# Kernel optimization log

Measured on AMD Instinct MI355X. Metric: run time of the kernel, lower is better.

## Reference

```python
import jax, jax.numpy as jnp
import numpy as np

CENTER_RADIUS = 2.5
TOPK = 13
IOU_WEIGHT = 3.0
BETA = 2.0
NUM_CLASSES = 80
BBOX_W = 2.0
BIG = 1e8
EPS = 1e-7
IMG = 1280


def pairwise_iou(boxes, gts):
    # boxes [N,4], gts [M,4] xyxy -> [N,M]
    lt = jnp.maximum(boxes[:, None, :2], gts[None, :, :2])
    rb = jnp.minimum(boxes[:, None, 2:], gts[None, :, 2:])
    wh = jnp.clip(rb - lt, 0.0)
    inter = wh[..., 0] * wh[..., 1]
    area_a = (boxes[:, 2] - boxes[:, 0]) * (boxes[:, 3] - boxes[:, 1])
    area_b = (gts[:, 2] - gts[:, 0]) * (gts[:, 3] - gts[:, 1])
    union = area_a[:, None] + area_b[None, :] - inter
    return inter / jnp.maximum(union, EPS)


def giou_elementwise(a, b):
    # a,b [N,4] xyxy -> [N]
    lt = jnp.maximum(a[:, :2], b[:, :2])
    rb = jnp.minimum(a[:, 2:], b[:, 2:])
    wh = jnp.clip(rb - lt, 0.0)
    inter = wh[:, 0] * wh[:, 1]
    area_a = (a[:, 2] - a[:, 0]) * (a[:, 3] - a[:, 1])
    area_b = (b[:, 2] - b[:, 0]) * (b[:, 3] - b[:, 1])
    union = area_a + area_b - inter
    iou = inter / jnp.maximum(union, EPS)
    elt = jnp.minimum(a[:, :2], b[:, :2])
    erb = jnp.maximum(a[:, 2:], b[:, 2:])
    ewh = jnp.clip(erb - elt, 0.0)
    enclose = ewh[:, 0] * ewh[:, 1]
    return iou - (enclose - union) / jnp.maximum(enclose, EPS)


def simota_assign(pred_scores, pred_boxes, points, strides, gt_boxes, gt_labels):
    N = points.shape[0]
    M = gt_boxes.shape[0]
    px, py = points[:, 0], points[:, 1]
    # Step 1: candidate selection (inside box OR inside center region)
    in_box = ((px[:, None] > gt_boxes[None, :, 0]) & (py[:, None] > gt_boxes[None, :, 1]) &
              (px[:, None] < gt_boxes[None, :, 2]) & (py[:, None] < gt_boxes[None, :, 3]))
    gcx = (gt_boxes[:, 0] + gt_boxes[:, 2]) * 0.5
    gcy = (gt_boxes[:, 1] + gt_boxes[:, 3]) * 0.5
    r = CENTER_RADIUS * strides[:, None]
    in_center = ((px[:, None] > gcx[None, :] - r) & (py[:, None] > gcy[None, :] - r) &
                 (px[:, None] < gcx[None, :] + r) & (py[:, None] < gcy[None, :] + r))
    is_cand = in_box | in_center          # [N,M]
    cand_any = is_cand.any(axis=1)        # [N]
    # Step 2: cost = BCE(prob, onehot) + w * (-log IoU)
    iou = pairwise_iou(pred_boxes, gt_boxes)  # [N,M]
    p = jnp.clip(pred_scores, 1e-6, 1.0 - 1e-6)
    log_p = jnp.log(p)
    log_1mp = jnp.log1p(-p)
    all_neg = -log_1mp.sum(axis=-1)       # [N] sum_c BCE(p_c, 0)
    cls_cost = all_neg[:, None] + log_1mp[:, gt_labels] - log_p[:, gt_labels]
    reg_cost = -jnp.log(iou + EPS)
    cost = cls_cost + IOU_WEIGHT * reg_cost
    cost = jnp.where(is_cand, cost, BIG)
    # Step 3: dynamic k from top-k IoUs over candidate points (candidates of any gt)
    iou_cand = jnp.where(cand_any[:, None], iou, 0.0)
    topk_ious, _ = jax.lax.top_k(iou_cand.T, TOPK)            # [M,TOPK]
    dyn_k = jnp.clip(topk_ious.sum(axis=-1).astype(jnp.int32), 1, None)  # [M], <= TOPK
    # Step 4: per-gt lowest-cost candidates; k_j entries, only valid (cost < BIG)
    neg_top, top_idx = jax.lax.top_k(-cost.T, TOPK)           # [M,TOPK]
    top_cost = -neg_top
    ranks = jnp.arange(TOPK)
    select = (ranks[None, :] < dyn_k[:, None]) & (top_cost < BIG)
    matching = jnp.zeros((N, M), bool).at[top_idx, jnp.arange(M)[:, None]].set(select)
    # Step 5: conflict resolution -> keep lowest-cost gt per point
    matched = matching.any(axis=1)
    best = jnp.argmin(jnp.where(matching, cost, jnp.inf), axis=1)  # [N]
    rows = jnp.arange(N)
    labels = jnp.where(matched, gt_labels[best], NUM_CLASSES)
    aboxes = jnp.where(matched[:, None], gt_boxes[best], 0.0)
    pos_iou = jnp.where(matched, iou[rows, best], 0.0)
    ascores = jnp.zeros((N, NUM_CLASSES), pred_scores.dtype).at[rows, gt_labels[best]].set(pos_iou)
    return labels, aboxes, ascores


def reference(pred_logits, pred_boxes, points, strides, gt_boxes, gt_labels):
    pred_scores = jax.nn.sigmoid(pred_logits)
    sg = jax.lax.stop_gradient
    labels, aboxes, ascores = simota_assign(sg(pred_scores), sg(pred_boxes),
                                            sg(points), sg(strides), sg(gt_boxes), gt_labels)
    labels, aboxes, ascores = sg(labels), sg(aboxes), sg(ascores)
    # Quality Focal Loss
    x, t = pred_logits, ascores
    bce = jnp.maximum(x, 0.0) - x * t + jnp.log1p(jnp.exp(-jnp.abs(x)))
    scale = jnp.abs(t - pred_scores) ** BETA
    n_pos_cls = jnp.maximum(1, (t > 0).sum()).astype(x.dtype)
    loss_cls = (scale * bce).sum() / n_pos_cls
    # GIoU loss over positives
    matched = labels < NUM_CLASSES
    g = giou_elementwise(pred_boxes, aboxes)
    n_pos = jnp.maximum(1, matched.sum()).astype(x.dtype)
    loss_box = jnp.where(matched, 1.0 - g, 0.0).sum() / n_pos
    return loss_cls + BBOX_W * loss_box


def setup_inputs() -> dict:
    key = jax.random.key(0)
    k1, k2, k3, k4, k5 = jax.random.split(key, 5)
    # multi-scale grid points for a 1280x1280 image, strides 8/16/32
    pts, strs = [], []
    for s in (8, 16, 32):
        n = IMG // s
        c = (jnp.arange(n, dtype=jnp.float32) + 0.5) * s
        yy, xx = jnp.meshgrid(c, c, indexing='ij')
        pts.append(jnp.stack([xx.ravel(), yy.ravel()], axis=-1))
        strs.append(jnp.full((n * n,), float(s), jnp.float32))
    points = jnp.concatenate(pts, axis=0)          # [33600,2]
    strides = jnp.concatenate(strs, axis=0)        # [33600]
    N = points.shape[0]
    pred_logits = jax.random.normal(k1, (N, NUM_CLASSES), jnp.float32) - 2.0
    # decode-style boxes: point +/- positive ltrb distances
    d = jax.random.uniform(k2, (N, 4), jnp.float32) * 64.0 + 1.0
    pred_boxes = jnp.stack([points[:, 0] - d[:, 0], points[:, 1] - d[:, 1],
                            points[:, 0] + d[:, 2], points[:, 1] + d[:, 3]], axis=-1)
    M = 256
    c = jax.random.uniform(k3, (M, 2), jnp.float32) * IMG
    wh = jax.random.uniform(k4, (M, 2), jnp.float32) * 200.0 + 8.0
    gt_boxes = jnp.concatenate([jnp.clip(c - wh / 2, 0, IMG), jnp.clip(c + wh / 2, 0, IMG)], axis=-1)
    gt_labels = jax.random.randint(k5, (M,), 0, NUM_CLASSES, jnp.int32)
    return {"pred_logits": pred_logits, "pred_boxes": pred_boxes, "points": points,
            "strides": strides, "gt_boxes": gt_boxes, "gt_labels": gt_labels}
```

## Files before the change

### kernel.cpp

```cpp
#include <hip/hip_runtime.h>
#include <cstdint>
#include <math.h>

#define NCLS 80
#define TKK 13
#define BIGC 100000000.0f
#define EPSC 1e-7f
#define CRAD 2.5f
#define MARGIN 66.0f
#define XCLP 13.815511f

__device__ __constant__ int   c_ln[3]   = {160, 80, 40};
__device__ __constant__ float c_ls[3]   = {8.0f, 16.0f, 32.0f};
__device__ __constant__ int   c_lbase[3]= {0, 25600, 32000};

__device__ __forceinline__ void sig_sp(float x, float& s, float& sp){
    float e = __expf(-fabsf(x));
    float L = __logf(1.0f + e);
    sp = fmaxf(x, 0.0f) + L;
    s = __fdividef((x >= 0.0f) ? 1.0f : e, 1.0f + e);
}

__global__ __launch_bounds__(256) void k_prep(
    const float* __restrict__ logits, const float* __restrict__ gt,
    int M, int N, int nbA4,
    unsigned long long* __restrict__ best, char* __restrict__ cand,
    float* __restrict__ comb_t, double* __restrict__ base_cls)
{
    int b = blockIdx.x;
    if (b < nbA4){
        int g = b * 256 + threadIdx.x;
        int n = g >> 2, p = g & 3;
        if (n >= N) return;
        const float4* lg4 = (const float4*)(logits + (size_t)n * NCLS + p * 20);
        float xs[20];
        float an = 0.0f;
        double bc = 0.0;
        #pragma unroll
        for (int q = 0; q < 5; q++){
            float4 v = lg4[q];
            xs[q*4+0] = v.x; xs[q*4+1] = v.y; xs[q*4+2] = v.z; xs[q*4+3] = v.w;
            #pragma unroll
            for (int k = 0; k < 4; k++){
                float x = xs[q*4+k];
                float s, sp;
                sig_sp(x, s, sp);
                an += fminf(sp, XCLP);
                bc += (double)((s * s) * sp);
            }
        }
        an += __shfl_down(an, 2, 4);
        an += __shfl_down(an, 1, 4);
        an = __shfl(an, 0, 4);
        bc += __shfl_down(bc, 2, 4);
        bc += __shfl_down(bc, 1, 4);
        #pragma unroll
        for (int q = 0; q < 20; q++){
            float xc = fminf(fmaxf(xs[q], -XCLP), XCLP);
            comb_t[(size_t)(p * 20 + q) * N + n] = an - xc;
        }
        if (p == 0){
            base_cls[n] = bc;
            best[n] = 0xFFFFFFFFFFFFFFFFull;
        }
    } else {
        int m = b - nbA4;
        int tid = threadIdx.x;
        float gx0 = gt[4*m], gy0 = gt[4*m+1], gx1 = gt[4*m+2], gy1 = gt[4*m+3];
        float cx = (gx0 + gx1) * 0.5f, cy = (gy0 + gy1) * 0.5f;
        for (int lvl = 0; lvl < 3; lvl++){
            int   ng = c_ln[lvl];
            float s  = c_ls[lvl];
            int   base = c_lbase[lvl];
            float r = CRAD * s;
            float xlo = fminf(gx0, cx - r), xhi = fmaxf(gx1, cx + r);
            float ylo = fminf(gy0, cy - r), yhi = fmaxf(gy1, cy + r);
            int j0 = max(0, (int)floorf(xlo / s - 0.5f));
            int j1 = min(ng - 1, (int)ceilf(xhi / s - 0.5f));
            int i0 = max(0, (int)floorf(ylo / s - 0.5f));
            int i1 = min(ng - 1, (int)ceilf(yhi / s - 0.5f));
            if (j1 < j0 || i1 < i0) continue;
            int w = j1 - j0 + 1;
            int cells = w * (i1 - i0 + 1);
            for (int c = tid; c < cells; c += 256){
                int ii = i0 + c / w, jj = j0 + c % w;
                float px = (jj + 0.5f) * s, py = (ii + 0.5f) * s;
                bool ib = (px > gx0) && (py > gy0) && (px < gx1) && (py < gy1);
                bool ic = (px > cx - r) && (py > cy - r) && (px < cx + r) && (py < cy + r);
                if (ib || ic) cand[base + ii * ng + jj] = 1;
            }
        }
    }
}

__global__ __launch_bounds__(256, 2) void k_assign(
    const float* __restrict__ pboxes, const float* __restrict__ comb_t,
    const float* __restrict__ gt, const int* __restrict__ glab,
    const char* __restrict__ cand,
    unsigned long long* __restrict__ best, int N)
{
    int m = blockIdx.x;
    int tid = threadIdx.x;
    int lane = tid & 63, wv = tid >> 6;

    float gx0 = gt[4*m], gy0 = gt[4*m+1], gx1 = gt[4*m+2], gy1 = gt[4*m+3];
    float areaB = (gx1 - gx0) * (gy1 - gy0);
    float cx = (gx0 + gx1) * 0.5f, cy = (gy0 + gy1) * 0.5f;
    int lab = glab[m];
    const float* __restrict__ combrow = comb_t + (size_t)lab * N;

    float liou[TKK];
    float lc[TKK]; int li[TKK];
    #pragma unroll
    for (int r = 0; r < TKK; r++){ liou[r] = 0.0f; lc[r] = INFINITY; li[r] = 0x7fffffff; }

    for (int lvl = 0; lvl < 3; lvl++){
        int   ng = c_ln[lvl];
        float s  = c_ls[lvl];
        int   base = c_lbase[lvl];
        float r = CRAD * s;
        float xlo = fminf(gx0 - MARGIN, cx - r), xhi = fmaxf(gx1 + MARGIN, cx + r);
        float ylo = fminf(gy0 - MARGIN, cy - r), yhi = fmaxf(gy1 + MARGIN, cy + r);
        int j0 = max(0, (int)floorf(xlo / s - 0.5f));
        int j1 = min(ng - 1, (int)ceilf(xhi / s - 0.5f));
        int i0 = max(0, (int)floorf(ylo / s - 0.5f));
        int i1 = min(ng - 1, (int)ceilf(yhi / s - 0.5f));
        if (j1 < j0 || i1 < i0) continue;
        int w = j1 - j0 + 1;
        int cells = w * (i1 - i0 + 1);
        for (int cb = wv * 64; cb < cells; cb += 1024){
            #pragma unroll
            for (int k = 0; k < 4; k++){
                int c = cb + k * 256 + lane;
                if (c >= cells) continue;
                int ii = i0 + (int)((unsigned)c / (unsigned)w);
                int jj = j0 + (int)((unsigned)c % (unsigned)w);
                int n = base + ii * ng + jj;

                float4 pb = ((const float4*)pboxes)[n];
                float comb = combrow[n];
                char  cd   = cand[n];

                float ltx = fmaxf(pb.x, gx0), lty = fmaxf(pb.y, gy0);
                float rbx = fminf(pb.z, gx1), rby = fminf(pb.w, gy1);
                float ww = fmaxf(rbx - ltx, 0.0f), hh = fmaxf(rby - lty, 0.0f);
                float inter = ww * hh;
                float areaA = (pb.z - pb.x) * (pb.w - pb.y);
                float uni = areaA + areaB - inter;
                float iou = inter / fmaxf(uni, EPSC);

                float ioum = cd ? iou : 0.0f;
                if (ioum > liou[TKK-1]){
                    float v = ioum;
                    #pragma unroll
                    for (int j = 0; j < TKK; j++){
                        float a = liou[j];
                        bool ins = (v > a);
                        liou[j] = ins ? v : a;
                        v = ins ? a : v;
                    }
                }

                float px = (jj + 0.5f) * s, py = (ii + 0.5f) * s;
                bool ib = (px > gx0) && (py > gy0) && (px < gx1) && (py < gy1);
                bool ic = (px > cx - r) && (py > cy - r) && (px < cx + r) && (py < cy + r);
                float cost = comb + 3.0f * (-__logf(iou + EPSC));
                bool top = (ib || ic) &&
                           ((cost < lc[TKK-1]) || (cost == lc[TKK-1] && n < li[TKK-1]));
                if (top){
                    float v = cost; int ix = n;
                    #pragma unroll
                    for (int j = 0; j < TKK; j++){
                        float a = lc[j]; int ai = li[j];
                        bool ins = (v < a) || (v == a && ix < ai);
                        lc[j] = ins ? v : a;  li[j] = ins ? ix : ai;
                        v = ins ? a : v;      ix = ins ? ai : ix;
                    }
                }
            }
        }
    }

    __shared__ float s_iou[4*TKK];
    __shared__ float s_cv[4*TKK];
    __shared__ int   s_ci[4*TKK];
    __shared__ float s_topc[TKK];
    __shared__ int   s_topi[TKK];
    __shared__ int   s_dynk;

    for (int r = 0; r < TKK; r++){
        float v = liou[0]; int o = lane;
        #pragma unroll
        for (int off = 32; off > 0; off >>= 1){
            float ov = __shfl_down(v, off);
            int   oo = __shfl_down(o, off);
            if (ov > v){ v = ov; o = oo; }
        }
        v = __shfl(v, 0); o = __shfl(o, 0);
        if (lane == 0) s_iou[wv*TKK + r] = v;
        if (v <= 0.0f){
            if (lane == 0) for (int rr = r+1; rr < TKK; rr++) s_iou[wv*TKK + rr] = 0.0f;
            break;
        }
        if (lane == o){
            #pragma unroll
            for (int j = 0; j < TKK-1; j++) liou[j] = liou[j+1];
            liou[TKK-1] = 0.0f;
        }
    }
    for (int r = 0; r < TKK; r++){
        float v = lc[0]; int ix = li[0]; int o = lane;
        #pragma unroll
        for (int off = 32; off > 0; off >>= 1){
            float ov = __shfl_down(v, off);
            int  oix = __shfl_down(ix, off);
            int   oo = __shfl_down(o, off);
            if (ov < v || (ov == v && oix < ix)){ v = ov; ix = oix; o = oo; }
        }
        v = __shfl(v, 0); ix = __shfl(ix, 0); o = __shfl(o, 0);
        if (lane == 0){ s_cv[wv*TKK + r] = v; s_ci[wv*TKK + r] = ix; }
        if (v == INFINITY){
            if (lane == 0) for (int rr = r+1; rr < TKK; rr++){
                s_cv[wv*TKK + rr] = INFINITY; s_ci[wv*TKK + rr] = 0x7fffffff;
            }
            break;
        }
        if (lane == o){
            #pragma unroll
            for (int j = 0; j < TKK-1; j++){ lc[j] = lc[j+1]; li[j] = li[j+1]; }
            lc[TKK-1] = INFINITY; li[TKK-1] = 0x7fffffff;
        }
    }
    __syncthreads();

    if (wv == 0){
        float v = (lane < 4*TKK) ? s_iou[lane] : 0.0f;
        float isum = 0.0f;
        for (int r = 0; r < TKK; r++){
            float x = v; int o = lane;
            #pragma unroll
            for (int off = 32; off > 0; off >>= 1){
                float ox = __shfl_down(x, off);
                int   oo = __shfl_down(o, off);
                if (ox > x){ x = ox; o = oo; }
            }
            x = __shfl(x, 0); o = __shfl(o, 0);
            if (x <= 0.0f) break;
            isum += x;
            if (lane == o) v = 0.0f;
        }
        if (lane == 0){
            int dynk = (int)isum;
            if (dynk < 1) dynk = 1;
            if (dynk > TKK) dynk = TKK;
            s_dynk = dynk;
        }
    } else if (wv == 1){
        float cv; int ci;
        if (lane < 4*TKK){ cv = s_cv[lane]; ci = s_ci[lane]; }
        else { cv = INFINITY; ci = 0x7fffffff; }
        for (int r = 0; r < TKK; r++){
            float x = cv; int xi = ci; int o = lane;
            #pragma unroll
            for (int off = 32; off > 0; off >>= 1){
                float ox = __shfl_down(x, off);
                int  oxi = __shfl_down(xi, off);
                int   oo = __shfl_down(o, off);
                if (ox < x || (ox == x && oxi < xi)){ x = ox; xi = oxi; o = oo; }
            }
            x = __shfl(x, 0); xi = __shfl(xi, 0); o = __shfl(o, 0);
            if (lane == 0){ s_topc[r] = x; s_topi[r] = xi; }
            if (x == INFINITY){
                if (lane == 0) for (int rr = r+1; rr < TKK; rr++){
                    s_topc[rr] = INFINITY; s_topi[rr] = 0x7fffffff;
                }
                break;
            }
            if (lane == o){ cv = INFINITY; ci = 0x7fffffff; }
        }
    }
    __syncthreads();

    if (tid < s_dynk){
        float c = s_topc[tid];
        int   i = s_topi[tid];
        if (c < BIGC && i < 0x7fffffff){
            unsigned u = __float_as_uint(c);
            u = (u & 0x80000000u) ? ~u : (u | 0x80000000u);
            unsigned long long key = ((unsigned long long)u << 32) | (unsigned)m;
            atomicMin(best + i, key);
        }
    }
}

__global__ __launch_bounds__(256) void k_loss(
    const float* __restrict__ logits, const float* __restrict__ pboxes,
    const float* __restrict__ gt, const int* __restrict__ glab,
    const unsigned long long* __restrict__ best,
    const double* __restrict__ base_cls,
    double* __restrict__ accd, int* __restrict__ acci,
    int N, int nblocks, float* __restrict__ out)
{
    int n = blockIdx.x * 256 + threadIdx.x;
    int tid = threadIdx.x;
    int lane = tid & 63, wv = tid >> 6;
    double scls = 0.0, sbox = 0.0;
    int cm = 0, cp = 0;

    if (n < N){
        scls = base_cls[n];
        unsigned long long b = best[n];
        if (b != 0xFFFFFFFFFFFFFFFFull){
            int m = (int)(b & 0xFFFFFFFFu);
            int lab = glab[m];
            float4 pb = ((const float4*)pboxes)[n];
            float gx0 = gt[4*m], gy0 = gt[4*m+1], gx1 = gt[4*m+2], gy1 = gt[4*m+3];
            float ltx = fmaxf(pb.x, gx0), lty = fmaxf(pb.y, gy0);
            float rbx = fminf(pb.z, gx1), rby = fminf(pb.w, gy1);
            float w = fmaxf(rbx - ltx, 0.0f), h = fmaxf(rby - lty, 0.0f);
            float inter = w * h;
            float areaA = (pb.z - pb.x) * (pb.w - pb.y);
            float areaB = (gx1 - gx0) * (gy1 - gy0);
            float uni = areaA + areaB - inter;
            float iou = inter / fmaxf(uni, EPSC);
            float eltx = fminf(pb.x, gx0), elty = fminf(pb.y, gy0);
            float erbx = fmaxf(pb.z, gx1), erby = fmaxf(pb.w, gy1);
            float ew = fmaxf(erbx - eltx, 0.0f), eh = fmaxf(erby - elty, 0.0f);
            float enc = ew * eh;
            float giou = iou - (enc - uni) / fmaxf(enc, EPSC);
            sbox = (double)(1.0f - giou);
            cm = 1;
            cp = (iou > 0.0f) ? 1 : 0;
            float x = logits[(size_t)n * NCLS + lab];
            float s, spv;
            sig_sp(x, s, spv);
            float bcet = spv - x * iou;
            float d = iou - s;
            scls = scls - (double)((s * s) * spv) + (double)((d * d) * bcet);
        }
    }

    #pragma unroll
    for (int off = 32; off > 0; off >>= 1){
        scls += __shfl_down(scls, off);
        sbox += __shfl_down(sbox, off);
        cm   += __shfl_down(cm, off);
        cp   += __shfl_down(cp, off);
    }
    __shared__ double sd0[4];
    __shared__ double sd1[4];
    __shared__ int    si0[4];
    __shared__ int    si1[4];
    if (lane == 0){ sd0[wv] = scls; sd1[wv] = sbox; si0[wv] = cm; si1[wv] = cp; }
    __syncthreads();
    if (tid == 0){
        double a0 = 0.0, a1 = 0.0; int c0 = 0, c1 = 0;
        #pragma unroll
        for (int q = 0; q < 4; q++){ a0 += sd0[q]; a1 += sd1[q]; c0 += si0[q]; c1 += si1[q]; }
        atomicAdd(&accd[0], a0);
        atomicAdd(&accd[1], a1);
        atomicAdd(&acci[0], c0);
        atomicAdd(&acci[1], c1);
        __threadfence();
        int donec = atomicAdd(&acci[2], 1);
        if (donec == nblocks - 1){
            double A0 = atomicAdd(&accd[0], 0.0);
            double A1 = atomicAdd(&accd[1], 0.0);
            int C0 = atomicAdd(&acci[0], 0);
            int C1 = atomicAdd(&acci[1], 0);
            if (C0 < 1) C0 = 1;
            if (C1 < 1) C1 = 1;
            out[0] = (float)(A0 / (double)C1 + 2.0 * A1 / (double)C0);
        }
    }
}

extern "C" void kernel_launch(void* const* d_in, const int* in_sizes, int n_in,
                              void* d_out, int out_size, void* d_ws, size_t ws_size,
                              hipStream_t stream) {
    const float* logits  = (const float*)d_in[0];
    const float* pboxes  = (const float*)d_in[1];
    const float* gtb     = (const float*)d_in[4];
    const int*   glab    = (const int*)d_in[5];

    int N = in_sizes[3];
    int M = in_sizes[5];

    char* ws = (char*)d_ws;
    size_t off = 0;
    unsigned long long* best = (unsigned long long*)(ws + off); off += (size_t)8 * N;
    double* base_cls = (double*)(ws + off); off += (size_t)8 * N;
    float*  comb_t   = (float*)(ws + off);  off += (size_t)4 * NCLS * N;
    size_t zstart = off;
    char*   cand = (char*)(ws + off);       off += (size_t)N;
    off = (off + 15) & ~(size_t)15;
    double* accd = (double*)(ws + off);     off += 16;
    int*    acci = (int*)(ws + off);        off += 16;
    size_t zlen = off - zstart;

    hipMemsetAsync(ws + zstart, 0, zlen, stream);

    int nbA4 = (4 * N + 255) / 256;
    int nbL  = (N + 255) / 256;
    k_prep<<<nbA4 + M, 256, 0, stream>>>(logits, gtb, M, N, nbA4,
                                         best, cand, comb_t, base_cls);
    k_assign<<<M, 256, 0, stream>>>(pboxes, comb_t, gtb, glab, cand, best, N);
    k_loss<<<nbL, 256, 0, stream>>>(logits, pboxes, gtb, glab, best, base_cls,
                                    accd, acci, N, nbL, (float*)d_out);
}
```

Baseline: 121.7 us.

## Replace iterative top-k shuffle extraction with bitonic lane merges and drop memset

The per-gt top-k reduction of IoU and cost lists across lanes and waves used to be thirteen rounds of argmax or argmin shuffles. It is now a bitonic merge network over 16-wide padded lists using xor shuffles, and the cross-wave merge works the same way. The hipMemsetAsync on the cand and accumulator region is removed; the accumulators are now zeroed inside k_prep, and the mask test becomes cd==1. k_assign launch bounds drop to one block per SM, which allows more registers for the larger unrolled arrays. The risk is that cand is no longer explicitly cleared each call, so stale workspace contents could be read if k_prep does not overwrite them.

Result: slower. 168.2 us (+38.2%).

```diff
diff --git a/kernel.cpp b/kernel.cpp
--- a/kernel.cpp
+++ b/kernel.cpp
@@ -4,11 +4,13 @@
 
 #define NCLS 80
 #define TKK 13
+#define KK 16
 #define BIGC 100000000.0f
 #define EPSC 1e-7f
 #define CRAD 2.5f
 #define MARGIN 66.0f
 #define XCLP 13.815511f
+#define AW 4
 
 __device__ __constant__ int   c_ln[3]   = {160, 80, 40};
 __device__ __constant__ float c_ls[3]   = {8.0f, 16.0f, 32.0f};
@@ -21,15 +23,64 @@
     s = __fdividef((x >= 0.0f) ? 1.0f : e, 1.0f + e);
 }
 
+__device__ __forceinline__ void merge_iou_level(float A[KK], int mask){
+    float B[KK];
+    #pragma unroll
+    for (int j = 0; j < KK; j++) B[j] = __shfl_xor(A[j], mask);
+    #pragma unroll
+    for (int j = 0; j < KK; j++) A[j] = fmaxf(A[j], B[KK-1-j]);
+    #pragma unroll
+    for (int d = 8; d > 0; d >>= 1){
+        #pragma unroll
+        for (int j = 0; j < KK; j++){
+            if ((j & d) == 0){
+                float hi = fmaxf(A[j], A[j|d]);
+                float lo = fminf(A[j], A[j|d]);
+                A[j] = hi; A[j|d] = lo;
+            }
+        }
+    }
+}
+__device__ __forceinline__ void merge_cost_level(float V[KK], int I[KK], int mask){
+    float Bv[KK]; int Bi[KK];
+    #pragma unroll
+    for (int j = 0; j < KK; j++){ Bv[j] = __shfl_xor(V[j], mask); Bi[j] = __shfl_xor(I[j], mask); }
+    #pragma unroll
+    for (int j = 0; j < KK; j++){
+        float bv = Bv[KK-1-j]; int bi = Bi[KK-1-j];
+        bool t = (V[j] < bv) || (V[j] == bv && I[j] < bi);
+        V[j] = t ? V[j] : bv;
+        I[j] = t ? I[j] : bi;
+    }
+    #pragma unroll
+    for (int d = 8; d > 0; d >>= 1){
+        #pragma unroll
+        for (int j = 0; j < KK; j++){
+            if ((j & d) == 0){
+                int k2 = j | d;
+                bool t = (V[j] < V[k2]) || (V[j] == V[k2] && I[j] < I[k2]);
+                float lv = t ? V[j] : V[k2];  int lix = t ? I[j] : I[k2];
+                float hv = t ? V[k2] : V[j];  int hix = t ? I[k2] : I[j];
+                V[j] = lv; I[j] = lix; V[k2] = hv; I[k2] = hix;
+            }
+        }
+    }
+}
+
 __global__ __launch_bounds__(256) void k_prep(
     const float* __restrict__ logits, const float* __restrict__ gt,
     int M, int N, int nbA4,
     unsigned long long* __restrict__ best, char* __restrict__ cand,
-    float* __restrict__ comb_t, double* __restrict__ base_cls)
+    float* __restrict__ comb_t, double* __restrict__ base_cls,
+    double* __restrict__ accd, int* __restrict__ acci)
 {
     int b = blockIdx.x;
     if (b < nbA4){
         int g = b * 256 + threadIdx.x;
+        if (g == 0){
+            accd[0] = 0.0; accd[1] = 0.0;
+            acci[0] = 0; acci[1] = 0; acci[2] = 0;
+        }
         int n = g >> 2, p = g & 3;
         if (n >= N) return;
         const float4* lg4 = (const float4*)(logits + (size_t)n * NCLS + p * 20);
@@ -93,7 +144,7 @@
     }
 }
 
-__global__ __launch_bounds__(256, 2) void k_assign(
+__global__ __launch_bounds__(256, 1) void k_assign(
     const float* __restrict__ pboxes, const float* __restrict__ comb_t,
     const float* __restrict__ gt, const int* __restrict__ glab,
     const char* __restrict__ cand,
@@ -149,7 +200,7 @@
                 float uni = areaA + areaB - inter;
                 float iou = inter / fmaxf(uni, EPSC);
 
-                float ioum = cd ? iou : 0.0f;
+                float ioum = (cd == 1) ? iou : 0.0f;
                 if (ioum > liou[TKK-1]){
                     float v = ioum;
                     #pragma unroll
@@ -181,102 +232,67 @@
         }
     }
 
-    __shared__ float s_iou[4*TKK];
-    __shared__ float s_cv[4*TKK];
-    __shared__ int   s_ci[4*TKK];
+    __shared__ float s_iou[AW*KK];
+    __shared__ float s_cv[AW*KK];
+    __shared__ int   s_ci[AW*KK];
     __shared__ float s_topc[TKK];
     __shared__ int   s_topi[TKK];
     __shared__ int   s_dynk;
 
-    for (int r = 0; r < TKK; r++){
-        float v = liou[0]; int o = lane;
-        #pragma unroll
-        for (int off = 32; off > 0; off >>= 1){
-            float ov = __shfl_down(v, off);
-            int   oo = __shfl_down(o, off);
-            if (ov > v){ v = ov; o = oo; }
-        }
-        v = __shfl(v, 0); o = __shfl(o, 0);
-        if (lane == 0) s_iou[wv*TKK + r] = v;
-        if (v <= 0.0f){
-            if (lane == 0) for (int rr = r+1; rr < TKK; rr++) s_iou[wv*TKK + rr] = 0.0f;
-            break;
-        }
-        if (lane == o){
-            #pragma unroll
-            for (int j = 0; j < TKK-1; j++) liou[j] = liou[j+1];
-            liou[TKK-1] = 0.0f;
-        }
-    }
-    for (int r = 0; r < TKK; r++){
-        float v = lc[0]; int ix = li[0]; int o = lane;
-        #pragma unroll
-        for (int off = 32; off > 0; off >>= 1){
-            float ov = __shfl_down(v, off);
-            int  oix = __shfl_down(ix, off);
-            int   oo = __shfl_down(o, off);
-            if (ov < v || (ov == v && oix < ix)){ v = ov; ix = oix; o = oo; }
-        }
-        v = __shfl(v, 0); ix = __shfl(ix, 0); o = __shfl(o, 0);
-        if (lane == 0){ s_cv[wv*TKK + r] = v; s_ci[wv*TKK + r] = ix; }
-        if (v == INFINITY){
-            if (lane == 0) for (int rr = r+1; rr < TKK; rr++){
-                s_cv[wv*TKK + rr] = INFINITY; s_ci[wv*TKK + rr] = 0x7fffffff;
-            }
-            break;
-        }
-        if (lane == o){
-            #pragma unroll
-            for (int j = 0; j < TKK-1; j++){ lc[j] = lc[j+1]; li[j] = li[j+1]; }
-            lc[TKK-1] = INFINITY; li[TKK-1] = 0x7fffffff;
+    {
+        float fi[KK];
+        #pragma unroll
+        for (int j = 0; j < TKK; j++) fi[j] = liou[j];
+        #pragma unroll
+        for (int j = TKK; j < KK; j++) fi[j] = 0.0f;
+        #pragma unroll
+        for (int mask = 1; mask < 64; mask <<= 1) merge_iou_level(fi, mask);
+        if (lane == 0){
+            #pragma unroll
+            for (int j = 0; j < KK; j++) s_iou[wv*KK + j] = fi[j];
+        }
+    }
+    {
+        float fv[KK]; int fx[KK];
+        #pragma unroll
+        for (int j = 0; j < TKK; j++){ fv[j] = lc[j]; fx[j] = li[j]; }
+        #pragma unroll
+        for (int j = TKK; j < KK; j++){ fv[j] = INFINITY; fx[j] = 0x7fffffff; }
+        #pragma unroll
+        for (int mask = 1; mask < 64; mask <<= 1) merge_cost_level(fv, fx, mask);
+        if (lane == 0){
+            #pragma unroll
+            for (int j = 0; j < KK; j++){ s_cv[wv*KK + j] = fv[j]; s_ci[wv*KK + j] = fx[j]; }
         }
     }
     __syncthreads();
 
     if (wv == 0){
-        float v = (lane < 4*TKK) ? s_iou[lane] : 0.0f;
-        float isum = 0.0f;
-        for (int r = 0; r < TKK; r++){
-            float x = v; int o = lane;
-            #pragma unroll
-            for (int off = 32; off > 0; off >>= 1){
-                float ox = __shfl_down(x, off);
-                int   oo = __shfl_down(o, off);
-                if (ox > x){ x = ox; o = oo; }
-            }
-            x = __shfl(x, 0); o = __shfl(o, 0);
-            if (x <= 0.0f) break;
-            isum += x;
-            if (lane == o) v = 0.0f;
-        }
+        float A[KK];
+        int w4 = lane & (AW - 1);
+        #pragma unroll
+        for (int j = 0; j < KK; j++) A[j] = s_iou[w4*KK + j];
+        merge_iou_level(A, 1);
+        merge_iou_level(A, 2);
         if (lane == 0){
+            float isum = 0.0f;
+            #pragma unroll
+            for (int j = 0; j < TKK; j++) isum += A[j];
             int dynk = (int)isum;
             if (dynk < 1) dynk = 1;
             if (dynk > TKK) dynk = TKK;
             s_dynk = dynk;
         }
     } else if (wv == 1){
-        float cv; int ci;
-        if (lane < 4*TKK){ cv = s_cv[lane]; ci = s_ci[lane]; }
-        else { cv = INFINITY; ci = 0x7fffffff; }
-        for (int r = 0; r < TKK; r++){
-            float x = cv; int xi = ci; int o = lane;
-            #pragma unroll
-            for (int off = 32; off > 0; off >>= 1){
-                float ox = __shfl_down(x, off);
-                int  oxi = __shfl_down(xi, off);
-                int   oo = __shfl_down(o, off);
-                if (ox < x || (ox == x && oxi < xi)){ x = ox; xi = oxi; o = oo; }
-            }
-            x = __shfl(x, 0); xi = __shfl(xi, 0); o = __shfl(o, 0);
-            if (lane == 0){ s_topc[r] = x; s_topi[r] = xi; }
-            if (x == INFINITY){
-                if (lane == 0) for (int rr = r+1; rr < TKK; rr++){
-                    s_topc[rr] = INFINITY; s_topi[rr] = 0x7fffffff;
-                }
-                break;
-            }
-            if (lane == o){ cv = INFINITY; ci = 0x7fffffff; }
+        float V[KK]; int I[KK];
+        int w4 = lane & (AW - 1);
+        #pragma unroll
+        for (int j = 0; j < KK; j++){ V[j] = s_cv[w4*KK + j]; I[j] = s_ci[w4*KK + j]; }
+        merge_cost_level(V, I, 1);
+        merge_cost_level(V, I, 2);
+        if (lane == 0){
+            #pragma unroll
+            for (int j = 0; j < TKK; j++){ s_topc[j] = V[j]; s_topi[j] = I[j]; }
         }
     }
     __syncthreads();
@@ -391,19 +407,15 @@
     unsigned long long* best = (unsigned long long*)(ws + off); off += (size_t)8 * N;
     double* base_cls = (double*)(ws + off); off += (size_t)8 * N;
     float*  comb_t   = (float*)(ws + off);  off += (size_t)4 * NCLS * N;
-    size_t zstart = off;
     char*   cand = (char*)(ws + off);       off += (size_t)N;
     off = (off + 15) & ~(size_t)15;
     double* accd = (double*)(ws + off);     off += 16;
     int*    acci = (int*)(ws + off);        off += 16;
-    size_t zlen = off - zstart;
-
-    hipMemsetAsync(ws + zstart, 0, zlen, stream);
 
     int nbA4 = (4 * N + 255) / 256;
     int nbL  = (N + 255) / 256;
     k_prep<<<nbA4 + M, 256, 0, stream>>>(logits, gtb, M, N, nbA4,
-                                         best, cand, comb_t, base_cls);
+                                         best, cand, comb_t, base_cls, accd, acci);
     k_assign<<<M, 256, 0, stream>>>(pboxes, comb_t, gtb, glab, cand, best, N);
     k_loss<<<nbL, 256, 0, stream>>>(logits, pboxes, gtb, glab, best, base_cls,
                                     accd, acci, N, nbL, (float*)d_out);
```

## Transpose logits through shared memory for coalesced comb_t writes and drop memset

Applied to the files above, without the earlier changes.

The logit-prep blocks now each handle 64 points. They stage the logits in a padded shared-memory tile and then write the transposed comb_t rows, so each wavefront stores 64 consecutive floats instead of short 16-point runs. The separate hipMemsetAsync is removed: block 0 now zeroes the accumulators inside k_prep. The candidate flag test becomes an explicit ==1 check, which suggests the cand buffer is no longer zeroed on the host side. In exchange, the code assumes N is a multiple of 64, drops the bounds check, and depends on cand being reset correctly somewhere else.

After: 119.7 us. No clear change (-1.6%).

```diff
diff --git a/kernel.cpp b/kernel.cpp
--- a/kernel.cpp
+++ b/kernel.cpp
@@ -23,15 +23,22 @@
 
 __global__ __launch_bounds__(256) void k_prep(
     const float* __restrict__ logits, const float* __restrict__ gt,
-    int M, int N, int nbA4,
+    int M, int N, int nbA,
     unsigned long long* __restrict__ best, char* __restrict__ cand,
-    float* __restrict__ comb_t, double* __restrict__ base_cls)
+    float* __restrict__ comb_t, double* __restrict__ base_cls,
+    double* __restrict__ accd, int* __restrict__ acci)
 {
     int b = blockIdx.x;
-    if (b < nbA4){
-        int g = b * 256 + threadIdx.x;
-        int n = g >> 2, p = g & 3;
-        if (n >= N) return;
+    if (b < nbA){
+        __shared__ float t[64][81];
+        __shared__ float s_an[64];
+        int tid = threadIdx.x;
+        if (b == 0 && tid == 0){
+            accd[0] = 0.0; accd[1] = 0.0;
+            acci[0] = 0; acci[1] = 0; acci[2] = 0;
+        }
+        int nl = tid >> 2, p = tid & 3;
+        int n = b * 64 + nl;
         const float4* lg4 = (const float4*)(logits + (size_t)n * NCLS + p * 20);
         float xs[20];
         float an = 0.0f;
@@ -49,22 +56,30 @@
                 bc += (double)((s * s) * sp);
             }
         }
+        #pragma unroll
+        for (int q = 0; q < 20; q++) t[nl][p * 20 + q] = xs[q];
         an += __shfl_down(an, 2, 4);
         an += __shfl_down(an, 1, 4);
-        an = __shfl(an, 0, 4);
         bc += __shfl_down(bc, 2, 4);
         bc += __shfl_down(bc, 1, 4);
-        #pragma unroll
-        for (int q = 0; q < 20; q++){
-            float xc = fminf(fmaxf(xs[q], -XCLP), XCLP);
-            comb_t[(size_t)(p * 20 + q) * N + n] = an - xc;
-        }
         if (p == 0){
+            s_an[nl] = an;
             base_cls[n] = bc;
             best[n] = 0xFFFFFFFFFFFFFFFFull;
         }
+        __syncthreads();
+        int lane = tid & 63, wv = tid >> 6;
+        int n0 = b * 64;
+        float av = s_an[lane];
+        #pragma unroll 5
+        for (int it = 0; it < 20; it++){
+            int c = it * 4 + wv;
+            float x = t[lane][c];
+            float xc = fminf(fmaxf(x, -XCLP), XCLP);
+            comb_t[(size_t)c * N + n0 + lane] = av - xc;
+        }
     } else {
-        int m = b - nbA4;
+        int m = b - nbA;
         int tid = threadIdx.x;
         float gx0 = gt[4*m], gy0 = gt[4*m+1], gx1 = gt[4*m+2], gy1 = gt[4*m+3];
         float cx = (gx0 + gx1) * 0.5f, cy = (gy0 + gy1) * 0.5f;
@@ -149,7 +164,7 @@
                 float uni = areaA + areaB - inter;
                 float iou = inter / fmaxf(uni, EPSC);
 
-                float ioum = cd ? iou : 0.0f;
+                float ioum = (cd == 1) ? iou : 0.0f;
                 if (ioum > liou[TKK-1]){
                     float v = ioum;
                     #pragma unroll
@@ -391,19 +406,15 @@
     unsigned long long* best = (unsigned long long*)(ws + off); off += (size_t)8 * N;
     double* base_cls = (double*)(ws + off); off += (size_t)8 * N;
     float*  comb_t   = (float*)(ws + off);  off += (size_t)4 * NCLS * N;
-    size_t zstart = off;
     char*   cand = (char*)(ws + off);       off += (size_t)N;
     off = (off + 15) & ~(size_t)15;
     double* accd = (double*)(ws + off);     off += 16;
     int*    acci = (int*)(ws + off);        off += 16;
-    size_t zlen = off - zstart;
-
-    hipMemsetAsync(ws + zstart, 0, zlen, stream);
-
-    int nbA4 = (4 * N + 255) / 256;
-    int nbL  = (N + 255) / 256;
-    k_prep<<<nbA4 + M, 256, 0, stream>>>(logits, gtb, M, N, nbA4,
-                                         best, cand, comb_t, base_cls);
+
+    int nbA = N / 64;
+    int nbL = (N + 255) / 256;
+    k_prep<<<nbA + M, 256, 0, stream>>>(logits, gtb, M, N, nbA,
+                                        best, cand, comb_t, base_cls, accd, acci);
     k_assign<<<M, 256, 0, stream>>>(pboxes, comb_t, gtb, glab, cand, best, N);
     k_loss<<<nbL, 256, 0, stream>>>(logits, pboxes, gtb, glab, best, base_cls,
                                     accd, acci, N, nbL, (float*)d_out);
```
